# Performance work log

Hardware: AMD Instinct MI355X
Metric: run time of the kernel (lower is better)

The kernel has to match this reference:

```python
import jax, jax.numpy as jnp
import numpy as np

T, N, C, L = 256, 64, 4096, 32
BLANK = 0
NEG = -1e30  # effective log(0)


def setup_inputs() -> dict:
    key = jax.random.key(0)
    k1, k2 = jax.random.split(key)
    preds = jax.random.normal(k1, (T, N, C), dtype=jnp.float32)
    # labels in [1, C): never equal to blank index 0
    targets = jax.random.randint(k2, (N * L,), 1, C, dtype=jnp.int32)
    pred_lengths = jnp.full((N,), T, dtype=jnp.int32)
    target_lengths = jnp.full((N,), L, dtype=jnp.int32)
    return {"preds": preds, "targets": targets,
            "pred_lengths": pred_lengths, "target_lengths": target_lengths}


def _ctc_loss(log_probs, targets2d, pred_lengths, target_lengths):
    # log_probs: (T, N, C); targets2d: (N, L)
    T_, N_, _ = log_probs.shape
    L_ = targets2d.shape[1]
    S = 2 * L_ + 1
    # extended label sequence: blank, l1, blank, l2, ..., blank  -> (N, S)
    ext = jnp.full((N_, S), BLANK, dtype=targets2d.dtype)
    ext = ext.at[:, 1::2].set(targets2d)
    # lp_ext[t, n, s] = log_probs[t, n, ext[n, s]]  -> (T, N, S)
    lp_ext = log_probs[:, jnp.arange(N_)[:, None], ext]
    s_idx = jnp.arange(S)
    # positions beyond this sample's extended length are invalid
    valid_s = s_idx[None, :] < (2 * target_lengths[:, None] + 1)  # (N, S)
    # skip (s-2 -> s) transition allowed only for non-blank labels that differ
    # from the label two positions back
    skip_ok = (s_idx[None, :] >= 2) & (ext != BLANK) & (ext != jnp.roll(ext, 2, axis=1))

    alpha0 = jnp.full((N_, S), NEG, dtype=log_probs.dtype)
    alpha0 = alpha0.at[:, 0].set(lp_ext[0, :, 0])
    alpha0 = alpha0.at[:, 1].set(jnp.where(target_lengths > 0, lp_ext[0, :, 1], NEG))
    alpha0 = jnp.where(valid_s, alpha0, NEG)

    def step(alpha, inp):
        lp_t, t = inp
        a1 = alpha
        a2 = jnp.concatenate([jnp.full((N_, 1), NEG, alpha.dtype), alpha[:, :-1]], axis=1)
        a3 = jnp.concatenate([jnp.full((N_, 2), NEG, alpha.dtype), alpha[:, :-2]], axis=1)
        a3 = jnp.where(skip_ok, a3, NEG)
        comb = jnp.logaddexp(jnp.logaddexp(a1, a2), a3)
        new = jnp.where(valid_s, comb + lp_t, NEG)
        active = (t < pred_lengths)[:, None]  # freeze alpha past sample end
        return jnp.where(active, new, alpha), None

    alphaT, _ = jax.lax.scan(step, alpha0, (lp_ext[1:], jnp.arange(1, T_)))
    end = 2 * target_lengths  # index of final blank in extended sequence
    a_last = jnp.take_along_axis(alphaT, end[:, None], axis=1)[:, 0]
    a_prev = jnp.take_along_axis(alphaT, jnp.maximum(end - 1, 0)[:, None], axis=1)[:, 0]
    a_prev = jnp.where(target_lengths > 0, a_prev, NEG)
    nll = -jnp.logaddexp(a_last, a_prev)
    # zero_infinity=True: zero out infinite / degenerate losses
    nll = jnp.where(jnp.isfinite(nll) & (nll < 1e29), nll, 0.0)
    # reduction='mean': divide each loss by its target length, then batch mean
    return jnp.mean(nll / jnp.maximum(target_lengths, 1).astype(nll.dtype))


def reference(preds, targets, pred_lengths, target_lengths):
    log_probs = jax.nn.log_softmax(preds, axis=2)
    targets2d = targets.reshape(N, L)  # all target_lengths equal L here
    return _ctc_loss(log_probs, targets2d, pred_lengths, target_lengths)
```

## Files before the change

### kernel.cpp

```cpp
#include <hip/hip_runtime.h>
#include <math.h>

#define T_ 256
#define N_ 64
#define C_ 4096
#define L_ 32
#define SL_ 33
#define NEGV (-1e30f)

__device__ __forceinline__ float dpp_shr1(float x, float fill) {
    int r = __builtin_amdgcn_update_dpp(__float_as_int(fill), __float_as_int(x),
                                        0x138, 0xF, 0xF, false);
    return __int_as_float(r);
}

#define DPP_FMAX(v, ctrl) \
    fmaxf((v), __int_as_float(__builtin_amdgcn_update_dpp( \
        __float_as_int(v), __float_as_int(v), (ctrl), 0xF, 0xF, false)))

__device__ __forceinline__ float wred_max(float v) {
    #pragma unroll
    for (int o = 32; o > 0; o >>= 1) v = fmaxf(v, __shfl_xor(v, o));
    return v;
}
__device__ __forceinline__ float wred_sum(float v) {
    #pragma unroll
    for (int o = 32; o > 0; o >>= 1) v += __shfl_xor(v, o);
    return v;
}

__global__ __launch_bounds__(256) void k_row_lse(
        const float* __restrict__ preds, const int* __restrict__ targets,
        float* __restrict__ pmat, int* __restrict__ counter) {
    const int wv     = threadIdx.x >> 6;
    const int lane   = threadIdx.x & 63;
    const int row_id = (blockIdx.x << 2) | wv;
    if (blockIdx.x == 0 && threadIdx.x == 0) *counter = 0;
    const int n = row_id & (N_ - 1);
    const float* row = preds + (size_t)row_id * C_;

    float gv = 0.f;
    if (lane < SL_) {
        const int cls = (lane == 0) ? 0 : targets[n * L_ + (lane - 1)];
        gv = row[cls];
    }

    float4 v[16];
    #pragma unroll
    for (int k = 0; k < 16; ++k) v[k] = ((const float4*)row)[lane + (k << 6)];

    float m = v[0].x;
    #pragma unroll
    for (int k = 0; k < 16; ++k)
        m = fmaxf(m, fmaxf(fmaxf(v[k].x, v[k].y), fmaxf(v[k].z, v[k].w)));
    m = wred_max(m);

    float s = 0.f;
    #pragma unroll
    for (int k = 0; k < 16; ++k)
        s += __expf(v[k].x - m) + __expf(v[k].y - m)
           + __expf(v[k].z - m) + __expf(v[k].w - m);
    s = wred_sum(s);
    const float lse = m + __logf(s);

    if (lane < SL_) {
        const int t = row_id >> 6;
        pmat[((size_t)n * T_ + t) * SL_ + lane] = __expf(gv - lse);
    }
}

__global__ __launch_bounds__(256) void k_ctc_scan(
        const float* __restrict__ pmat, const int* __restrict__ targets,
        const int* __restrict__ plen, const int* __restrict__ tlen,
        float* __restrict__ partial, int* __restrict__ counter,
        float* __restrict__ out) {
    __shared__ __align__(16) float lds[(T_ + 16) * SL_];
    const int n = blockIdx.x;
    const int tid = threadIdx.x;
    const float4* src = (const float4*)(pmat + (size_t)n * T_ * SL_);
    float4* dst = (float4*)lds;
    for (int i = tid; i < (T_ * SL_) / 4; i += 256) dst[i] = src[i];
    __syncthreads();
    if (tid >= 64) return;

    const int lane = tid;
    const int tl = tlen[n];
    const int pl = plen[n];
    const int ends = 2 * tl;
    const bool odd = (lane & 1);
    const int slot   = odd ? 1 + (lane >> 1) : 0;
    const int cls    = odd ? targets[n * L_ + (lane >> 1)] : 0;
    const int clsm2  = (odd && lane >= 2) ? targets[n * L_ + (lane >> 1) - 1] : 0;
    const bool skip  = odd && (lane >= 2) && (cls != 0) && (cls != clsm2);
    const bool valid   = lane < 2 * tl + 1;
    const bool valid64 = (2 * tl + 1) > 64;

    float A = 0.f, B = 0.f;
    int esum = 0;
    if (lane == 0) A = lds[0];
    if (lane == 1 && tl > 0) A = lds[1];

    float pf_s[8], pf_b[8];
    #pragma unroll
    for (int j = 0; j < 8; ++j) {
        pf_s[j] = valid   ? lds[(1 + j) * SL_ + slot] : 0.f;
        pf_b[j] = valid64 ? lds[(1 + j) * SL_]        : 0.f;
    }

    for (int t = 1; t <= T_; t += 8) {
        #pragma unroll
        for (int j = 0; j < 8; ++j) {
            const float p_s = pf_s[j];
            const float p_b = pf_b[j];
            pf_s[j] = valid   ? lds[(t + 8 + j) * SL_ + slot] : 0.f;
            pf_b[j] = valid64 ? lds[(t + 8 + j) * SL_]        : 0.f;

            const float A2 = dpp_shr1(A, 0.f);
            float A3 = dpp_shr1(A2, 0.f);
            A3 = skip ? A3 : 0.f;
            const float sum3 = (A + A2) + A3;
            const float nA = sum3 * p_s;
            const float nB = (B + A) * p_b;
            if (t + j < pl) { A = nA; B = nB; }
        }
        if (t + 7 < pl) {
            float mx = fmaxf(A, (lane == 63) ? B : 0.f);
            mx = DPP_FMAX(mx, 0x111);
            mx = DPP_FMAX(mx, 0x112);
            mx = DPP_FMAX(mx, 0x114);
            mx = DPP_FMAX(mx, 0x118);
            mx = DPP_FMAX(mx, 0x142);
            mx = DPP_FMAX(mx, 0x143);
            const float mxu = __int_as_float(
                __builtin_amdgcn_readlane(__float_as_int(mx), 63));
            if (mxu > 0.f) {
                const int eb = (__float_as_int(mxu) >> 23) & 255;
                const float scale = __int_as_float((254 - eb) << 23);
                A *= scale; B *= scale;
                esum += eb - 127;
            }
        }
    }

    const float a_last = (ends >= 64) ? __shfl(B, 63) : __shfl(A, ends);
    float a_prev = __shfl(A, (ends > 0) ? (ends - 1) : 0);
    if (tl <= 0) a_prev = 0.f;
    float nll = -(__logf(a_last + a_prev) + (float)esum * 0.69314718056f);
    if (!(isfinite(nll) && nll < 1e29f)) nll = 0.f;
    if (lane == 0) partial[n] = nll / (float)((tl > 0) ? tl : 1);

    __threadfence();
    int done = 0;
    if (lane == 0) done = atomicAdd(counter, 1);
    done = __shfl(done, 0);
    if (done == N_ - 1) {
        __threadfence();
        float v = partial[lane];
        v = wred_sum(v);
        if (lane == 0) out[0] = v * (1.0f / (float)N_);
    }
}

extern "C" void kernel_launch(void* const* d_in, const int* in_sizes, int n_in,
                              void* d_out, int out_size, void* d_ws, size_t ws_size,
                              hipStream_t stream) {
    const float* preds   = (const float*)d_in[0];
    const int*   targets = (const int*)d_in[1];
    const int*   plen    = (const int*)d_in[2];
    const int*   tlen    = (const int*)d_in[3];

    float* pmat    = (float*)d_ws;
    float* partial = pmat + (size_t)N_ * T_ * SL_;
    int*   counter = (int*)(partial + N_);

    k_row_lse<<<(T_ * N_) / 4, 256, 0, stream>>>(preds, targets, pmat, counter);
    k_ctc_scan<<<N_, 256, 0, stream>>>(pmat, targets, plen, tlen, partial,
                                       counter, (float*)d_out);
}
```

Measured before the change: 383.4 us.

## Fuse row log-softmax and CTC scan into one kernel via ticket counter

Merges the row log-sum-exp kernel and the CTC alpha scan kernel into a single launch. Each block takes a ticket from an atomic counter, and the last 64 blocks to finish become scan blocks, which spin until every block has published its pmat rows through system-coherent stores. This removes one kernel launch and the gap between the kernels. The cost is a memset launch, a spin-wait, and a larger LDS allocation on every block, which may lower occupancy for the row phase.

```diff
diff --git a/kernel.cpp b/kernel.cpp
--- a/kernel.cpp
+++ b/kernel.cpp
@@ -6,7 +6,7 @@
 #define C_ 4096
 #define L_ 32
 #define SL_ 33
-#define NEGV (-1e30f)
+#define NBLK (T_ * N_ / 4)
 
 __device__ __forceinline__ float dpp_shr1(float x, float fill) {
     int r = __builtin_amdgcn_update_dpp(__float_as_int(fill), __float_as_int(x),
@@ -29,13 +29,22 @@
     return v;
 }
 
-__global__ __launch_bounds__(256) void k_row_lse(
+__device__ __forceinline__ void store_agent_f32(float* p, float v) {
+    asm volatile("global_store_dword %0, %1, off sc0 sc1"
+                 :: "v"(p), "v"(v) : "memory");
+}
+
+__global__ __launch_bounds__(256) void k_fused(
         const float* __restrict__ preds, const int* __restrict__ targets,
-        float* __restrict__ pmat, int* __restrict__ counter) {
+        const int* __restrict__ plen, const int* __restrict__ tlen,
+        float* __restrict__ pmat, float* __restrict__ partial,
+        int* counter, float* __restrict__ out) {
+    __shared__ __align__(16) float lds[(T_ + 16) * SL_];
+    __shared__ int s_ticket;
+
     const int wv     = threadIdx.x >> 6;
     const int lane   = threadIdx.x & 63;
     const int row_id = (blockIdx.x << 2) | wv;
-    if (blockIdx.x == 0 && threadIdx.x == 0) *counter = 0;
     const int n = row_id & (N_ - 1);
     const float* row = preds + (size_t)row_id * C_;
 
@@ -65,40 +74,49 @@
 
     if (lane < SL_) {
         const int t = row_id >> 6;
-        pmat[((size_t)n * T_ + t) * SL_ + lane] = __expf(gv - lse);
+        store_agent_f32(&pmat[((size_t)n * T_ + t) * SL_ + lane],
+                        __expf(gv - lse));
     }
-}
 
-__global__ __launch_bounds__(256) void k_ctc_scan(
-        const float* __restrict__ pmat, const int* __restrict__ targets,
-        const int* __restrict__ plen, const int* __restrict__ tlen,
-        float* __restrict__ partial, int* __restrict__ counter,
-        float* __restrict__ out) {
-    __shared__ __align__(16) float lds[(T_ + 16) * SL_];
-    const int n = blockIdx.x;
-    const int tid = threadIdx.x;
-    const float4* src = (const float4*)(pmat + (size_t)n * T_ * SL_);
-    float4* dst = (float4*)lds;
-    for (int i = tid; i < (T_ * SL_) / 4; i += 256) dst[i] = src[i];
+    asm volatile("s_waitcnt vmcnt(0)" ::: "memory");
     __syncthreads();
-    if (tid >= 64) return;
+    if (threadIdx.x == 0) s_ticket = atomicAdd(counter, 1);
+    __syncthreads();
+    const int ticket = s_ticket;
+    if (ticket < NBLK - N_) return;
 
-    const int lane = tid;
-    const int tl = tlen[n];
-    const int pl = plen[n];
+    const int myn = ticket - (NBLK - N_);
+    const int tl = tlen[myn];
+    const int pl = plen[myn];
+
+    if (threadIdx.x == 0) {
+        while (__hip_atomic_load(counter, __ATOMIC_RELAXED,
+                                 __HIP_MEMORY_SCOPE_AGENT) < NBLK)
+            __builtin_amdgcn_s_sleep(1);
+    }
+    __syncthreads();
+    __threadfence();
+
+    const float4* src = (const float4*)(pmat + (size_t)myn * T_ * SL_);
+    float4* dst4 = (float4*)lds;
+    for (int i = threadIdx.x; i < (T_ * SL_) / 4; i += 256) dst4[i] = src[i];
+    __syncthreads();
+    if (threadIdx.x >= 64) return;
+
+    const int sl   = threadIdx.x;
     const int ends = 2 * tl;
-    const bool odd = (lane & 1);
-    const int slot   = odd ? 1 + (lane >> 1) : 0;
-    const int cls    = odd ? targets[n * L_ + (lane >> 1)] : 0;
-    const int clsm2  = (odd && lane >= 2) ? targets[n * L_ + (lane >> 1) - 1] : 0;
-    const bool skip  = odd && (lane >= 2) && (cls != 0) && (cls != clsm2);
-    const bool valid   = lane < 2 * tl + 1;
+    const bool odd = (sl & 1);
+    const int slot   = odd ? 1 + (sl >> 1) : 0;
+    const int cls    = odd ? targets[myn * L_ + (sl >> 1)] : 0;
+    const int clsm2  = (odd && sl >= 2) ? targets[myn * L_ + (sl >> 1) - 1] : 0;
+    const bool skip  = odd && (sl >= 2) && (cls != 0) && (cls != clsm2);
+    const bool valid   = sl < 2 * tl + 1;
     const bool valid64 = (2 * tl + 1) > 64;
 
     float A = 0.f, B = 0.f;
     int esum = 0;
-    if (lane == 0) A = lds[0];
-    if (lane == 1 && tl > 0) A = lds[1];
+    if (sl == 0) A = lds[0];
+    if (sl == 1 && tl > 0) A = lds[1];
 
     float pf_s[8], pf_b[8];
     #pragma unroll
@@ -124,7 +142,7 @@
             if (t + j < pl) { A = nA; B = nB; }
         }
         if (t + 7 < pl) {
-            float mx = fmaxf(A, (lane == 63) ? B : 0.f);
+            float mx = fmaxf(A, (sl == 63) ? B : 0.f);
             mx = DPP_FMAX(mx, 0x111);
             mx = DPP_FMAX(mx, 0x112);
             mx = DPP_FMAX(mx, 0x114);
@@ -147,17 +165,17 @@
     if (tl <= 0) a_prev = 0.f;
     float nll = -(__logf(a_last + a_prev) + (float)esum * 0.69314718056f);
     if (!(isfinite(nll) && nll < 1e29f)) nll = 0.f;
-    if (lane == 0) partial[n] = nll / (float)((tl > 0) ? tl : 1);
+    if (sl == 0) partial[myn] = nll / (float)((tl > 0) ? tl : 1);
 
     __threadfence();
     int done = 0;
-    if (lane == 0) done = atomicAdd(counter, 1);
+    if (sl == 0) done = atomicAdd(counter, 1);
     done = __shfl(done, 0);
-    if (done == N_ - 1) {
+    if (done == NBLK + N_ - 1) {
         __threadfence();
-        float v = partial[lane];
-        v = wred_sum(v);
-        if (lane == 0) out[0] = v * (1.0f / (float)N_);
+        float pv = partial[sl];
+        pv = wred_sum(pv);
+        if (sl == 0) out[0] = pv * (1.0f / (float)N_);
     }
 }
 
@@ -173,7 +191,7 @@
     float* partial = pmat + (size_t)N_ * T_ * SL_;
     int*   counter = (int*)(partial + N_);
 
-    k_row_lse<<<(T_ * N_) / 4, 256, 0, stream>>>(preds, targets, pmat, counter);
-    k_ctc_scan<<<N_, 256, 0, stream>>>(pmat, targets, plen, tlen, partial,
-                                       counter, (float*)d_out);
+    hipMemsetAsync(counter, 0, sizeof(int), stream);
+    k_fused<<<NBLK, 256, 0, stream>>>(preds, targets, plen, tlen, pmat,
+                                      partial, counter, (float*)d_out);
 }
```

Measured after the change: 406.3 us. 1.06x slower.

## Process each softmax row with a full 256-thread block instead of one wave

Applied to the files above, without the earlier changes.

The row log-sum-exp kernel now assigns one 4096-element row to a whole 256-thread block, with each thread loading four float4s instead of one wave per row loading sixteen per lane. Max and sum reductions gain a cross-wave step through shared memory with two barriers. The aim is to cut per-thread register pressure and raise memory-level parallelism and occupancy when streaming the 256 MB input, at the cost of four times as many blocks and the extra synchronization.

```diff
diff --git a/kernel.cpp b/kernel.cpp
--- a/kernel.cpp
+++ b/kernel.cpp
@@ -6,7 +6,6 @@
 #define C_ 4096
 #define L_ 32
 #define SL_ 33
-#define NEGV (-1e30f)
 
 __device__ __forceinline__ float dpp_shr1(float x, float fill) {
     int r = __builtin_amdgcn_update_dpp(__float_as_int(fill), __float_as_int(x),
@@ -32,38 +31,46 @@
 __global__ __launch_bounds__(256) void k_row_lse(
         const float* __restrict__ preds, const int* __restrict__ targets,
         float* __restrict__ pmat, int* __restrict__ counter) {
-    const int wv     = threadIdx.x >> 6;
-    const int lane   = threadIdx.x & 63;
-    const int row_id = (blockIdx.x << 2) | wv;
-    if (blockIdx.x == 0 && threadIdx.x == 0) *counter = 0;
+    __shared__ float red[8];
+    const int row_id = blockIdx.x;
+    const int tid  = threadIdx.x;
+    const int wv   = tid >> 6;
+    const int lane = tid & 63;
+    if (row_id == 0 && tid == 0) *counter = 0;
     const int n = row_id & (N_ - 1);
     const float* row = preds + (size_t)row_id * C_;
 
     float gv = 0.f;
-    if (lane < SL_) {
+    if (wv == 0 && lane < SL_) {
         const int cls = (lane == 0) ? 0 : targets[n * L_ + (lane - 1)];
         gv = row[cls];
     }
 
-    float4 v[16];
+    float4 v[4];
     #pragma unroll
-    for (int k = 0; k < 16; ++k) v[k] = ((const float4*)row)[lane + (k << 6)];
+    for (int j = 0; j < 4; ++j) v[j] = ((const float4*)row)[tid + (j << 8)];
 
     float m = v[0].x;
     #pragma unroll
-    for (int k = 0; k < 16; ++k)
-        m = fmaxf(m, fmaxf(fmaxf(v[k].x, v[k].y), fmaxf(v[k].z, v[k].w)));
+    for (int j = 0; j < 4; ++j)
+        m = fmaxf(m, fmaxf(fmaxf(v[j].x, v[j].y), fmaxf(v[j].z, v[j].w)));
     m = wred_max(m);
+    if (lane == 0) red[wv] = m;
+    __syncthreads();
+    m = fmaxf(fmaxf(red[0], red[1]), fmaxf(red[2], red[3]));
 
     float s = 0.f;
     #pragma unroll
-    for (int k = 0; k < 16; ++k)
-        s += __expf(v[k].x - m) + __expf(v[k].y - m)
-           + __expf(v[k].z - m) + __expf(v[k].w - m);
+    for (int j = 0; j < 4; ++j)
+        s += __expf(v[j].x - m) + __expf(v[j].y - m)
+           + __expf(v[j].z - m) + __expf(v[j].w - m);
     s = wred_sum(s);
+    if (lane == 0) red[4 + wv] = s;
+    __syncthreads();
+    s = (red[4] + red[5]) + (red[6] + red[7]);
     const float lse = m + __logf(s);
 
-    if (lane < SL_) {
+    if (wv == 0 && lane < SL_) {
         const int t = row_id >> 6;
         pmat[((size_t)n * T_ + t) * SL_ + lane] = __expf(gv - lse);
     }
@@ -173,7 +180,7 @@
     float* partial = pmat + (size_t)N_ * T_ * SL_;
     int*   counter = (int*)(partial + N_);
 
-    k_row_lse<<<(T_ * N_) / 4, 256, 0, stream>>>(preds, targets, pmat, counter);
+    k_row_lse<<<T_ * N_, 256, 0, stream>>>(preds, targets, pmat, counter);
     k_ctc_scan<<<N_, 256, 0, stream>>>(pmat, targets, plen, tlen, partial,
                                        counter, (float*)d_out);
 }
```

After: 379.0 us. About the same (-1.2%).
